# Kernel optimization log

Hardware: AMD Instinct MI355X
Metric: run time of the kernel (lower is better)

Reference implementation:

```python
import jax, jax.numpy as jnp
import numpy as np
from jax import lax

N, CI, CO, H, W = 2, 256, 256, 64, 64
K, G, DIL, PAD, STRIDE = 3, 8, 1, 1, 1
P = K * K
CG = CO // G  # group channels = 32


def setup_inputs() -> dict:
    key = jax.random.key(0)
    ks = jax.random.split(key, 24)
    r = lambda i, shape, s=1.0: jax.random.normal(ks[i], shape, jnp.float32) * s
    u = lambda i, shape: jax.random.uniform(ks[i], shape, jnp.float32, 0.5, 1.5)
    return dict(
        x=r(0, (N, CI, H, W)),
        conv1_w=r(1, (CO, CI), CI ** -0.5),
        bn1_g=u(2, (CO,)), bn1_b=r(3, (CO,), 0.1), bn1_m=r(4, (CO,), 0.1), bn1_v=u(5, (CO,)),
        inproj_w=r(6, (CO, CO), CO ** -0.5), inproj_b=r(7, (CO,), 0.02),
        dw_w=r(8, (CO, 1, K, K), 0.2), dw_b=r(9, (CO,), 0.02),
        ln_g=u(10, (CO,)), ln_b=r(11, (CO,), 0.02),
        off_w=r(12, (CO, G * P * 2), CO ** -0.5), off_b=jnp.zeros((G * P * 2,), jnp.float32),
        mask_w=r(13, (CO, G * P), CO ** -0.5), mask_b=jnp.zeros((G * P,), jnp.float32),
        outproj_w=r(14, (CO, CO), CO ** -0.5), outproj_b=r(15, (CO,), 0.02),
        bn2_g=u(16, (CO,)), bn2_b=r(17, (CO,), 0.1), bn2_m=r(18, (CO,), 0.1), bn2_v=u(19, (CO,)),
    )


def _bn(x, g, b, m, v, eps):
    # inference-mode BatchNorm2d on NCHW
    return (x - m[:, None, None]) * (g[:, None, None] * lax.rsqrt(v[:, None, None] + eps)) + b[:, None, None]


def _dcn_core(t, offset, mask):
    # t: (N,H,W,C) projected input; offset: (N,H,W,G*P*2); mask: (N,H,W,G,P) softmaxed
    xp = jnp.pad(t, ((0, 0), (PAD, PAD), (PAD, PAD), (0, 0)))
    H_, W_ = H + 2 * PAD, W + 2 * PAD
    # reference points (sample centers), normalized to padded size
    ry = ((DIL * (K - 1)) / 2 + 0.5 + STRIDE * jnp.arange(H, dtype=t.dtype)) / H_
    rx = ((DIL * (K - 1)) / 2 + 0.5 + STRIDE * jnp.arange(W, dtype=t.dtype)) / W_
    base = (DIL * (K - 1)) // 2
    gx = jnp.linspace(-base, -base + (K - 1) * DIL, K, dtype=t.dtype) / W_
    gy = jnp.linspace(-base, -base + (K - 1) * DIL, K, dtype=t.dtype) / H_
    gxx, gyy = jnp.meshgrid(gx, gy, indexing='ij')  # x varies along axis 0 (torch meshgrid order)
    grid = jnp.stack([gxx, gyy], -1).reshape(P, 2)  # (P,2)
    off = offset.reshape(N, H, W, G, P, 2) / jnp.array([W_, H_], t.dtype)
    loc_x = rx[None, None, :, None, None] + grid[:, 0][None, None, None, None] + off[..., 0]  # (N,H,W,G,P)
    loc_y = ry[None, :, None, None, None] + grid[:, 1][None, None, None, None] + off[..., 1]
    # grid_sample(align_corners=False): pixel = norm*size - 0.5
    px = jnp.transpose(loc_x * W_ - 0.5, (0, 3, 1, 2, 4)).reshape(N, G, H * W * P)
    py = jnp.transpose(loc_y * H_ - 0.5, (0, 3, 1, 2, 4)).reshape(N, G, H * W * P)
    # grouped channels-last image: (N,G,H_*W_,CG)
    xg = jnp.transpose(xp.reshape(N, H_, W_, G, CG), (0, 3, 1, 2, 4)).reshape(N, G, H_ * W_, CG)
    x0 = jnp.floor(px)
    y0 = jnp.floor(py)
    wx1 = px - x0
    wy1 = py - y0
    x0i = x0.astype(jnp.int32)
    y0i = y0.astype(jnp.int32)

    def corner(xi, yi, w):
        valid = (xi >= 0) & (xi <= W_ - 1) & (yi >= 0) & (yi <= H_ - 1)
        idx = jnp.clip(yi, 0, H_ - 1) * W_ + jnp.clip(xi, 0, W_ - 1)
        v = jnp.take_along_axis(xg, idx[..., None], axis=2)  # (N,G,M,CG)
        return v * jnp.where(valid, w, 0.0)[..., None]

    sampled = (corner(x0i, y0i, (1 - wx1) * (1 - wy1))
               + corner(x0i + 1, y0i, wx1 * (1 - wy1))
               + corner(x0i, y0i + 1, (1 - wx1) * wy1)
               + corner(x0i + 1, y0i + 1, wx1 * wy1))
    sampled = sampled.reshape(N, G, H * W, P, CG)
    mg = jnp.transpose(mask, (0, 3, 1, 2, 4)).reshape(N, G, H * W, P)
    out = jnp.einsum('nglpc,nglp->nglc', sampled, mg)
    return jnp.transpose(out, (0, 2, 1, 3)).reshape(N, H, W, G * CG)


def reference(x, conv1_w, bn1_g, bn1_b, bn1_m, bn1_v, inproj_w, inproj_b, dw_w, dw_b,
              ln_g, ln_b, off_w, off_b, mask_w, mask_b, outproj_w, outproj_b,
              bn2_g, bn2_b, bn2_m, bn2_v):
    # Conv(inc, ouc, k=1): 1x1 conv (no bias) + BN(eps=1e-3) + SiLU
    y = jnp.einsum('nchw,oc->nohw', x, conv1_w)
    y = jax.nn.silu(_bn(y, bn1_g, bn1_b, bn1_m, bn1_v, 1e-3))
    t = jnp.transpose(y, (0, 2, 3, 1))  # NHWC
    xproj = t @ inproj_w + inproj_b     # input_proj Linear
    # offset/mask branch: depthwise conv (k=3,s=1,p=1) -> LN over C -> GELU
    z = lax.conv_general_dilated(y, dw_w, (1, 1), ((PAD, PAD), (PAD, PAD)),
                                 feature_group_count=CO,
                                 dimension_numbers=('NCHW', 'OIHW', 'NCHW')) + dw_b[None, :, None, None]
    z = jnp.transpose(z, (0, 2, 3, 1))
    mu = jnp.mean(z, -1, keepdims=True)
    var = jnp.var(z, -1, keepdims=True)
    z = (z - mu) * lax.rsqrt(var + 1e-5) * ln_g + ln_b
    z = jax.nn.gelu(z, approximate=False)
    offset = z @ off_w + off_b  # (N,H,W,G*P*2)
    mask = jax.nn.softmax((z @ mask_w + mask_b).reshape(N, H, W, G, P), axis=-1)
    s = _dcn_core(xproj, offset, mask)
    s = s @ outproj_w + outproj_b  # output_proj Linear
    o = jnp.transpose(s, (0, 3, 1, 2))  # back to NCHW
    return jax.nn.silu(_bn(o, bn2_g, bn2_b, bn2_m, bn2_v, 1e-5))
```

## Files before the change

### kernel.cpp

```cpp
#include <hip/hip_runtime.h>
#include <hip/hip_fp16.h>
#include <math.h>

#define CC    256
#define HH    64
#define WW    64
#define HWSZ  4096
#define NPIX  8192
#define MT    16
#define TT    16
#define ASTR  264

typedef __attribute__((ext_vector_type(8))) _Float16 half8;
typedef __attribute__((ext_vector_type(4))) float f32x4;

__device__ __forceinline__ float silu_f(float x) { return x / (1.f + __expf(-x)); }

__device__ __forceinline__ short f2h(float f) {
    __half h = __float2half(f);
    return *reinterpret_cast<short*>(&h);
}
__device__ __forceinline__ unsigned h2u(float a, float b) {
    __half2 h = __floats2half2_rn(a, b);
    return *reinterpret_cast<unsigned*>(&h);
}
__device__ __forceinline__ __half2 u2h(unsigned v) { return *reinterpret_cast<__half2*>(&v); }
__device__ __forceinline__ unsigned h2raw(__half2 h) { return *reinterpret_cast<unsigned*>(&h); }
__device__ __forceinline__ float4 h2f4(uint2 u) {
    float2 a = __half22float2(u2h(u.x));
    float2 b = __half22float2(u2h(u.y));
    return make_float4(a.x, a.y, b.x, b.y);
}

__global__ void k_prep(const float* __restrict__ cw, const float* __restrict__ ipw,
                       const float* __restrict__ offw, const float* __restrict__ maskw,
                       const float* __restrict__ opw, const float* __restrict__ dww,
                       const float* __restrict__ offb, const float* __restrict__ maskb,
                       const float* __restrict__ g1, const float* __restrict__ b1,
                       const float* __restrict__ m1, const float* __restrict__ v1,
                       const float* __restrict__ g2, const float* __restrict__ b2,
                       const float* __restrict__ m2, const float* __restrict__ v2,
                       short* __restrict__ Wc1b, short* __restrict__ Wipb,
                       short* __restrict__ Whb, short* __restrict__ Wopb,
                       float* __restrict__ dwt,
                       float* __restrict__ bh, float* __restrict__ sc1, float* __restrict__ sh1,
                       float* __restrict__ sc2, float* __restrict__ sh2) {
    int o = blockIdx.x, c = threadIdx.x;
    Wc1b[o * CC + c] = f2h(cw[o * CC + c]);
    Wipb[o * CC + c] = f2h(ipw[c * CC + o]);
    float hv = 0.f;
    if (o < 144) hv = offw[c * 144 + o];
    else if (o < 216) hv = maskw[c * 72 + (o - 144)];
    Whb[o * CC + c] = f2h(hv);
    Wopb[o * CC + c] = f2h(opw[c * CC + o]);
    if (o < 9) dwt[o * CC + c] = dww[c * 9 + o];
    if (o == 0) {
        float bv = 0.f;
        if (c < 144) bv = offb[c];
        else if (c < 216) bv = maskb[c - 144];
        bh[c] = bv;
        float s1 = g1[c] * rsqrtf(v1[c] + 1e-3f);
        sc1[c] = s1; sh1[c] = b1[c] - m1[c] * s1;
        float s2 = g2[c] * rsqrtf(v2[c] + 1e-5f);
        sc2[c] = s2; sh2[c] = b2[c] - m2[c] * s2;
    }
}

__device__ __forceinline__ void gemm1(const short* As, const short* __restrict__ Wb,
                                      int lane, int n0, f32x4* acc) {
    const int m = lane & 15, q = lane >> 4;
#pragma unroll
    for (int kk = 0; kk < 8; ++kk) {
        int c0 = kk * 32 + q * 8;
        half8 a = *(const half8*)(As + m * ASTR + c0);
        half8 b = *(const half8*)(Wb + (size_t)(n0 + m) * CC + c0);
        *acc = __builtin_amdgcn_mfma_f32_16x16x32_f16(a, b, *acc, 0, 0, 0);
    }
}

__global__ __launch_bounds__(1024, 8) void k_conv_in(
        const float* __restrict__ x, const short* __restrict__ Wc1b,
        const short* __restrict__ Wipb, const float* __restrict__ sc1,
        const float* __restrict__ sh1, const float* __restrict__ ipb,
        short* __restrict__ ybf, short* __restrict__ xpb) {
    __shared__ __align__(16) short As[MT * ASTR];
    int tid = threadIdx.x, lane = tid & 63, wv = tid >> 6;
    int pix0 = blockIdx.x * MT;
    int n = pix0 >> 12, hw0 = pix0 & (HWSZ - 1);
    int n0 = wv * 16;
    const float* xn = x + (size_t)n * CC * HWSZ;
    {
        int c = tid >> 2, i4 = (tid & 3) * 4;
        float4 v = *(const float4*)(xn + (size_t)c * HWSZ + hw0 + i4);
        As[(i4 + 0) * ASTR + c] = f2h(v.x);
        As[(i4 + 1) * ASTR + c] = f2h(v.y);
        As[(i4 + 2) * ASTR + c] = f2h(v.z);
        As[(i4 + 3) * ASTR + c] = f2h(v.w);
    }
    __syncthreads();
    f32x4 acc = (f32x4){0.f, 0.f, 0.f, 0.f};
    gemm1(As, Wc1b, lane, n0, &acc);
    __syncthreads();
    int col = lane & 15, qr = (lane >> 4) * 4;
    int o = n0 + col;
    {
        float sc = sc1[o], sh = sh1[o];
#pragma unroll
        for (int r = 0; r < 4; ++r)
            As[(qr + r) * ASTR + o] = f2h(silu_f(acc[r] * sc + sh));
    }
    __syncthreads();
    *(uint2*)(ybf + (size_t)(pix0 + wv) * CC + lane * 4) =
        *(const uint2*)(As + wv * ASTR + lane * 4);
    acc = (f32x4){0.f, 0.f, 0.f, 0.f};
    gemm1(As, Wipb, lane, n0, &acc);
    __syncthreads();
    {
        float bo = ipb[o];
#pragma unroll
        for (int r = 0; r < 4; ++r)
            As[(qr + r) * ASTR + o] = f2h(acc[r] + bo);
    }
    __syncthreads();
    *(uint2*)(xpb + (size_t)(pix0 + wv) * CC + lane * 4) =
        *(const uint2*)(As + wv * ASTR + lane * 4);
}

__global__ __launch_bounds__(1024, 8) void k_tail(
        const short* __restrict__ ybf, const short* __restrict__ xpb,
        const float* __restrict__ dwt, const float* __restrict__ dwb,
        const float* __restrict__ lng, const float* __restrict__ lnb,
        const short* __restrict__ Whb, const float* __restrict__ bh,
        const short* __restrict__ Wopb, const float* __restrict__ opb,
        const float* __restrict__ sc2, const float* __restrict__ sh2,
        float* __restrict__ out) {
    __shared__ __align__(16) short As[TT * ASTR];
    __shared__ __align__(16) float buf[TT * 260];
    float* ml   = buf;
    float* loff = buf + 1216;
    float* xs   = buf;

    int tid = threadIdx.x, lane = tid & 63, wv = tid >> 6;
    int bid = blockIdx.x;
    int swz = ((bid & 7) << 6) | (bid >> 3);
    int pix0 = swz * TT;
    int n = pix0 >> 12, hw0 = pix0 & (HWSZ - 1);
    int h = hw0 >> 6, w0 = hw0 & 63;
    int c0 = lane * 4;
    int n0 = wv * 16;
    int col = lane & 15, qr = (lane >> 4) * 4;

    {
        float4 dwbv = *(const float4*)(dwb + c0);
        float4 lngv = *(const float4*)(lng + c0);
        float4 lnbv = *(const float4*)(lnb + c0);
        const short* yn = ybf + (size_t)n * HWSZ * CC;
        int pix = wv;
        int w = w0 + pix;
        float4 acc = dwbv;
#pragma unroll
        for (int ky = 0; ky < 3; ++ky) {
            int yy = h + ky - 1;
            int yc = min(max(yy, 0), HH - 1);
            float vy = (yy == yc) ? 1.f : 0.f;
#pragma unroll
            for (int kx = 0; kx < 3; ++kx) {
                int xx = w + kx - 1;
                int xc = min(max(xx, 0), WW - 1);
                float vm = vy * ((xx == xc) ? 1.f : 0.f);
                int t = ky * 3 + kx;
                float4 wt = *(const float4*)(dwt + t * CC + c0);
                float4 yv = h2f4(*(const uint2*)(yn + (size_t)((yc << 6) + xc) * CC + c0));
                acc.x += yv.x * wt.x * vm;
                acc.y += yv.y * wt.y * vm;
                acc.z += yv.z * wt.z * vm;
                acc.w += yv.w * wt.w * vm;
            }
        }
        float s1 = acc.x + acc.y + acc.z + acc.w;
        float s2 = acc.x * acc.x + acc.y * acc.y + acc.z * acc.z + acc.w * acc.w;
#pragma unroll
        for (int off = 32; off > 0; off >>= 1) {
            s1 += __shfl_xor(s1, off);
            s2 += __shfl_xor(s2, off);
        }
        float mu = s1 * (1.f / 256.f);
        float var = s2 * (1.f / 256.f) - mu * mu;
        float rs = rsqrtf(var + 1e-5f);
        float4 zv;
        zv.x = (acc.x - mu) * rs * lngv.x + lnbv.x;
        zv.y = (acc.y - mu) * rs * lngv.y + lnbv.y;
        zv.z = (acc.z - mu) * rs * lngv.z + lnbv.z;
        zv.w = (acc.w - mu) * rs * lngv.w + lnbv.w;
        zv.x = 0.5f * zv.x * (1.f + erff(zv.x * 0.70710678118654752f));
        zv.y = 0.5f * zv.y * (1.f + erff(zv.y * 0.70710678118654752f));
        zv.z = 0.5f * zv.z * (1.f + erff(zv.z * 0.70710678118654752f));
        zv.w = 0.5f * zv.w * (1.f + erff(zv.w * 0.70710678118654752f));
        *(uint2*)(As + pix * ASTR + c0) = make_uint2(h2u(zv.x, zv.y), h2u(zv.z, zv.w));
    }
    __syncthreads();

    {
        f32x4 acc = (f32x4){0.f, 0.f, 0.f, 0.f};
        gemm1(As, Whb, lane, n0, &acc);
        int o = n0 + col;
        float bo = bh[o];
#pragma unroll
        for (int r = 0; r < 4; ++r) {
            float v = acc[r] + bo;
            int pix = qr + r;
            if (o < 144) loff[pix * 144 + o] = v;
            else if (o < 216) ml[pix * 76 + (o - 144)] = v;
        }
    }
    __syncthreads();

    {
        int g  = lane >> 3;
        int ci = lane & 7;
        int gc0 = g * 32 + ci * 4;
        int pix = wv;
        int w = w0 + pix;
        float e9[9];
        {
            const float* row = ml + pix * 76 + g * 9;
            float mx = -1e30f;
#pragma unroll
            for (int p = 0; p < 9; ++p) { e9[p] = row[p]; mx = fmaxf(mx, e9[p]); }
            float ssum = 0.f;
#pragma unroll
            for (int p = 0; p < 9; ++p) { e9[p] = __expf(e9[p] - mx); ssum += e9[p]; }
            float inv = 1.f / ssum;
#pragma unroll
            for (int p = 0; p < 9; ++p) e9[p] *= inv;
        }
        const float* lp = loff + pix * 144 + g * 18;
        const short* xpn = xpb + (size_t)n * HWSZ * CC;
        __half2 a01 = u2h(0u), a23 = u2h(0u);
#pragma unroll
        for (int p = 0; p < 9; ++p) {
            float ox = lp[p * 2], oy = lp[p * 2 + 1];
            float px = (float)(w + p / 3) + ox;
            float py = (float)(h + p % 3) + oy;
            float fx = floorf(px), fy = floorf(py);
            float wx1 = px - fx, wy1 = py - fy;
            int x0 = (int)fx, y0 = (int)fy;
            int x1 = x0 + 1, y1 = y0 + 1;
            int xc0 = min(max(x0, 1), WW), xc1 = min(max(x1, 1), WW);
            int yc0 = min(max(y0, 1), HH), yc1 = min(max(y1, 1), HH);
            float vx0 = (x0 == xc0) ? 1.f : 0.f, vx1 = (x1 == xc1) ? 1.f : 0.f;
            float vy0 = (y0 == yc0) ? 1.f : 0.f, vy1 = (y1 == yc1) ? 1.f : 0.f;
            float mval = e9[p];
            float w00 = (1.f - wx1) * (1.f - wy1) * mval * vx0 * vy0;
            float w10 = wx1 * (1.f - wy1) * mval * vx1 * vy0;
            float w01 = (1.f - wx1) * wy1 * mval * vx0 * vy1;
            float w11 = wx1 * wy1 * mval * vx1 * vy1;
            uint2 u00 = *(const uint2*)(xpn + (size_t)(((yc0 - 1) << 6) + (xc0 - 1)) * CC + gc0);
            uint2 u10 = *(const uint2*)(xpn + (size_t)(((yc0 - 1) << 6) + (xc1 - 1)) * CC + gc0);
            uint2 u01 = *(const uint2*)(xpn + (size_t)(((yc1 - 1) << 6) + (xc0 - 1)) * CC + gc0);
            uint2 u11 = *(const uint2*)(xpn + (size_t)(((yc1 - 1) << 6) + (xc1 - 1)) * CC + gc0);
            __half2 W00 = __float2half2_rn(w00);
            __half2 W10 = __float2half2_rn(w10);
            __half2 W01 = __float2half2_rn(w01);
            __half2 W11 = __float2half2_rn(w11);
            a01 = __hfma2(u2h(u00.x), W00, a01); a23 = __hfma2(u2h(u00.y), W00, a23);
            a01 = __hfma2(u2h(u10.x), W10, a01); a23 = __hfma2(u2h(u10.y), W10, a23);
            a01 = __hfma2(u2h(u01.x), W01, a01); a23 = __hfma2(u2h(u01.y), W01, a23);
            a01 = __hfma2(u2h(u11.x), W11, a01); a23 = __hfma2(u2h(u11.y), W11, a23);
        }
        *(uint2*)(As + pix * ASTR + gc0) = make_uint2(h2raw(a01), h2raw(a23));
    }
    __syncthreads();

    {
        f32x4 acc = (f32x4){0.f, 0.f, 0.f, 0.f};
        gemm1(As, Wopb, lane, n0, &acc);
        int o = n0 + col;
        float bo = opb[o], sc = sc2[o], sh = sh2[o];
#pragma unroll
        for (int r = 0; r < 4; ++r)
            xs[(qr + r) * 260 + o] = silu_f((acc[r] + bo) * sc + sh);
    }
    __syncthreads();

    {
        int i4 = (tid & 3) * 4;
        int o = tid >> 2;
        float* on = out + (size_t)n * CC * HWSZ + hw0 + i4;
        float4 ov;
        ov.x = xs[(i4 + 0) * 260 + o];
        ov.y = xs[(i4 + 1) * 260 + o];
        ov.z = xs[(i4 + 2) * 260 + o];
        ov.w = xs[(i4 + 3) * 260 + o];
        *(float4*)(on + (size_t)o * HWSZ) = ov;
    }
}

extern "C" void kernel_launch(void* const* d_in, const int* in_sizes, int n_in,
                              void* d_out, int out_size, void* d_ws, size_t ws_size,
                              hipStream_t stream) {
    const float* x        = (const float*)d_in[0];
    const float* conv1_w  = (const float*)d_in[1];
    const float* bn1_g    = (const float*)d_in[2];
    const float* bn1_b    = (const float*)d_in[3];
    const float* bn1_m    = (const float*)d_in[4];
    const float* bn1_v    = (const float*)d_in[5];
    const float* inproj_w = (const float*)d_in[6];
    const float* inproj_b = (const float*)d_in[7];
    const float* dw_w     = (const float*)d_in[8];
    const float* dw_b     = (const float*)d_in[9];
    const float* ln_g     = (const float*)d_in[10];
    const float* ln_b     = (const float*)d_in[11];
    const float* off_w    = (const float*)d_in[12];
    const float* off_b    = (const float*)d_in[13];
    const float* mask_w   = (const float*)d_in[14];
    const float* mask_b   = (const float*)d_in[15];
    const float* outproj_w = (const float*)d_in[16];
    const float* outproj_b = (const float*)d_in[17];
    const float* bn2_g    = (const float*)d_in[18];
    const float* bn2_b    = (const float*)d_in[19];
    const float* bn2_m    = (const float*)d_in[20];
    const float* bn2_v    = (const float*)d_in[21];
    float* out = (float*)d_out;

    short* Wc1b = (short*)d_ws;
    short* Wipb = Wc1b + 65536;
    short* Whb  = Wipb + 65536;
    short* Wopb = Whb + 65536;
    float* fp   = (float*)(Wopb + 65536);
    float* dwt  = fp;
    float* bh   = dwt + 9 * CC;
    float* sc1  = bh + 256;
    float* sh1  = sc1 + 256;
    float* sc2  = sh1 + 256;
    float* sh2  = sc2 + 256;
    short* ybf  = (short*)(sh2 + 256);
    short* xpb  = ybf + (size_t)NPIX * CC;

    k_prep<<<dim3(CC), dim3(CC), 0, stream>>>(conv1_w, inproj_w, off_w, mask_w, outproj_w, dw_w,
                                              off_b, mask_b, bn1_g, bn1_b, bn1_m, bn1_v,
                                              bn2_g, bn2_b, bn2_m, bn2_v,
                                              Wc1b, Wipb, Whb, Wopb, dwt, bh, sc1, sh1, sc2, sh2);
    k_conv_in<<<dim3(NPIX / MT), dim3(1024), 0, stream>>>(x, Wc1b, Wipb, sc1, sh1, inproj_b, ybf, xpb);
    k_tail<<<dim3(NPIX / TT), dim3(1024), 0, stream>>>(ybf, xpb, dwt, dw_b, ln_g, ln_b,
                                                       Whb, bh, Wopb, outproj_b, sc2, sh2, out);
}
```

Before: 156.0 us.

## Split deformable sampling taps across lane pairs with wider loads and interior fast path

The bilinear sampling stage now gives each lane 8 channels (16-byte loads) and splits the 9 taps between two lanes (5 and 4), merging the partial sums with a shuffle-xor. The mask logits are stored at a 12-float stride so they can be read as float4, and the softmax max-subtraction is dropped. The depthwise conv also gains a branch-free path for blocks away from the image border. The aim is more memory parallelism per lane and fewer address and mask instructions, at the cost of dropping the overflow guard in the softmax and doing the fp16 cross-lane add.

```diff
diff --git a/kernel.cpp b/kernel.cpp
--- a/kernel.cpp
+++ b/kernel.cpp
@@ -137,7 +137,7 @@
     __shared__ __align__(16) short As[TT * ASTR];
     __shared__ __align__(16) float buf[TT * 260];
     float* ml   = buf;
-    float* loff = buf + 1216;
+    float* loff = buf + 1536;
     float* xs   = buf;
 
     int tid = threadIdx.x, lane = tid & 63, wv = tid >> 6;
@@ -158,23 +158,41 @@
         int pix = wv;
         int w = w0 + pix;
         float4 acc = dwbv;
-#pragma unroll
-        for (int ky = 0; ky < 3; ++ky) {
-            int yy = h + ky - 1;
-            int yc = min(max(yy, 0), HH - 1);
-            float vy = (yy == yc) ? 1.f : 0.f;
-#pragma unroll
-            for (int kx = 0; kx < 3; ++kx) {
-                int xx = w + kx - 1;
-                int xc = min(max(xx, 0), WW - 1);
-                float vm = vy * ((xx == xc) ? 1.f : 0.f);
-                int t = ky * 3 + kx;
-                float4 wt = *(const float4*)(dwt + t * CC + c0);
-                float4 yv = h2f4(*(const uint2*)(yn + (size_t)((yc << 6) + xc) * CC + c0));
-                acc.x += yv.x * wt.x * vm;
-                acc.y += yv.y * wt.y * vm;
-                acc.z += yv.z * wt.z * vm;
-                acc.w += yv.w * wt.w * vm;
+        bool inter = (h > 0) && (h < HH - 1) && (w0 > 0) && (w0 < WW - TT);
+        if (inter) {
+#pragma unroll
+            for (int ky = 0; ky < 3; ++ky) {
+#pragma unroll
+                for (int kx = 0; kx < 3; ++kx) {
+                    int t = ky * 3 + kx;
+                    float4 wt = *(const float4*)(dwt + t * CC + c0);
+                    int idx = ((h + ky - 1) << 6) + (w + kx - 1);
+                    float4 yv = h2f4(*(const uint2*)(yn + (size_t)idx * CC + c0));
+                    acc.x += yv.x * wt.x;
+                    acc.y += yv.y * wt.y;
+                    acc.z += yv.z * wt.z;
+                    acc.w += yv.w * wt.w;
+                }
+            }
+        } else {
+#pragma unroll
+            for (int ky = 0; ky < 3; ++ky) {
+                int yy = h + ky - 1;
+                int yc = min(max(yy, 0), HH - 1);
+                float vy = (yy == yc) ? 1.f : 0.f;
+#pragma unroll
+                for (int kx = 0; kx < 3; ++kx) {
+                    int xx = w + kx - 1;
+                    int xc = min(max(xx, 0), WW - 1);
+                    float vm = vy * ((xx == xc) ? 1.f : 0.f);
+                    int t = ky * 3 + kx;
+                    float4 wt = *(const float4*)(dwt + t * CC + c0);
+                    float4 yv = h2f4(*(const uint2*)(yn + (size_t)((yc << 6) + xc) * CC + c0));
+                    acc.x += yv.x * wt.x * vm;
+                    acc.y += yv.y * wt.y * vm;
+                    acc.z += yv.z * wt.z * vm;
+                    acc.w += yv.w * wt.w * vm;
+                }
             }
         }
         float s1 = acc.x + acc.y + acc.z + acc.w;
@@ -210,38 +228,42 @@
             float v = acc[r] + bo;
             int pix = qr + r;
             if (o < 144) loff[pix * 144 + o] = v;
-            else if (o < 216) ml[pix * 76 + (o - 144)] = v;
+            else if (o < 216) {
+                int mo = o - 144;
+                int mg = (mo * 7282) >> 16;
+                ml[pix * 96 + mg * 12 + (mo - mg * 9)] = v;
+            }
         }
     }
     __syncthreads();
 
     {
-        int g  = lane >> 3;
-        int ci = lane & 7;
-        int gc0 = g * 32 + ci * 4;
+        int g   = lane >> 3;
+        int ci  = lane & 7;
+        int cq  = ci & 3;
+        int par = ci >> 2;
+        int gc0 = g * 32 + cq * 8;
         int pix = wv;
         int w = w0 + pix;
-        float e9[9];
-        {
-            const float* row = ml + pix * 76 + g * 9;
-            float mx = -1e30f;
-#pragma unroll
-            for (int p = 0; p < 9; ++p) { e9[p] = row[p]; mx = fmaxf(mx, e9[p]); }
-            float ssum = 0.f;
-#pragma unroll
-            for (int p = 0; p < 9; ++p) { e9[p] = __expf(e9[p] - mx); ssum += e9[p]; }
-            float inv = 1.f / ssum;
-#pragma unroll
-            for (int p = 0; p < 9; ++p) e9[p] *= inv;
-        }
-        const float* lp = loff + pix * 144 + g * 18;
+        const float* row = ml + pix * 96 + g * 12;
+        float4 r0 = *(const float4*)(row);
+        float4 r1 = *(const float4*)(row + 4);
+        float e0 = __expf(r0.x), e1 = __expf(r0.y), e2 = __expf(r0.z);
+        float e3 = __expf(r0.w), e4 = __expf(r1.x), e5 = __expf(r1.y);
+        float e6 = __expf(r1.z), e7 = __expf(r1.w), e8 = __expf(row[8]);
+        float inv = 1.f / (e0 + e1 + e2 + e3 + e4 + e5 + e6 + e7 + e8);
+        float m0 = (par ? e5 : e0) * inv;
+        float m1 = (par ? e6 : e1) * inv;
+        float m2 = (par ? e7 : e2) * inv;
+        float m3 = (par ? e8 : e3) * inv;
+        float m4 = e4 * inv;
+        const float* lp = loff + pix * 144 + g * 18 + par * 10;
         const short* xpn = xpb + (size_t)n * HWSZ * CC;
-        __half2 a01 = u2h(0u), a23 = u2h(0u);
-#pragma unroll
-        for (int p = 0; p < 9; ++p) {
-            float ox = lp[p * 2], oy = lp[p * 2 + 1];
-            float px = (float)(w + p / 3) + ox;
-            float py = (float)(h + p % 3) + oy;
+        __half2 a0 = u2h(0u), a1 = u2h(0u), a2 = u2h(0u), a3 = u2h(0u);
+
+        auto dotap = [&](float ox, float oy, int tx, int ty, float mval) {
+            float px = (float)(w + tx) + ox;
+            float py = (float)(h + ty) + oy;
             float fx = floorf(px), fy = floorf(py);
             float wx1 = px - fx, wy1 = py - fy;
             int x0 = (int)fx, y0 = (int)fy;
@@ -250,25 +272,54 @@
             int yc0 = min(max(y0, 1), HH), yc1 = min(max(y1, 1), HH);
             float vx0 = (x0 == xc0) ? 1.f : 0.f, vx1 = (x1 == xc1) ? 1.f : 0.f;
             float vy0 = (y0 == yc0) ? 1.f : 0.f, vy1 = (y1 == yc1) ? 1.f : 0.f;
-            float mval = e9[p];
             float w00 = (1.f - wx1) * (1.f - wy1) * mval * vx0 * vy0;
             float w10 = wx1 * (1.f - wy1) * mval * vx1 * vy0;
             float w01 = (1.f - wx1) * wy1 * mval * vx0 * vy1;
             float w11 = wx1 * wy1 * mval * vx1 * vy1;
-            uint2 u00 = *(const uint2*)(xpn + (size_t)(((yc0 - 1) << 6) + (xc0 - 1)) * CC + gc0);
-            uint2 u10 = *(const uint2*)(xpn + (size_t)(((yc0 - 1) << 6) + (xc1 - 1)) * CC + gc0);
-            uint2 u01 = *(const uint2*)(xpn + (size_t)(((yc1 - 1) << 6) + (xc0 - 1)) * CC + gc0);
-            uint2 u11 = *(const uint2*)(xpn + (size_t)(((yc1 - 1) << 6) + (xc1 - 1)) * CC + gc0);
+            int i00 = (((yc0 - 1) << 6) + (xc0 - 1)) * CC + gc0;
+            int i10 = (((yc0 - 1) << 6) + (xc1 - 1)) * CC + gc0;
+            int i01 = (((yc1 - 1) << 6) + (xc0 - 1)) * CC + gc0;
+            int i11 = (((yc1 - 1) << 6) + (xc1 - 1)) * CC + gc0;
+            uint4 u00 = *(const uint4*)(xpn + i00);
+            uint4 u10 = *(const uint4*)(xpn + i10);
+            uint4 u01 = *(const uint4*)(xpn + i01);
+            uint4 u11 = *(const uint4*)(xpn + i11);
             __half2 W00 = __float2half2_rn(w00);
             __half2 W10 = __float2half2_rn(w10);
             __half2 W01 = __float2half2_rn(w01);
             __half2 W11 = __float2half2_rn(w11);
-            a01 = __hfma2(u2h(u00.x), W00, a01); a23 = __hfma2(u2h(u00.y), W00, a23);
-            a01 = __hfma2(u2h(u10.x), W10, a01); a23 = __hfma2(u2h(u10.y), W10, a23);
-            a01 = __hfma2(u2h(u01.x), W01, a01); a23 = __hfma2(u2h(u01.y), W01, a23);
-            a01 = __hfma2(u2h(u11.x), W11, a01); a23 = __hfma2(u2h(u11.y), W11, a23);
+            a0 = __hfma2(u2h(u00.x), W00, a0); a1 = __hfma2(u2h(u00.y), W00, a1);
+            a2 = __hfma2(u2h(u00.z), W00, a2); a3 = __hfma2(u2h(u00.w), W00, a3);
+            a0 = __hfma2(u2h(u10.x), W10, a0); a1 = __hfma2(u2h(u10.y), W10, a1);
+            a2 = __hfma2(u2h(u10.z), W10, a2); a3 = __hfma2(u2h(u10.w), W10, a3);
+            a0 = __hfma2(u2h(u01.x), W01, a0); a1 = __hfma2(u2h(u01.y), W01, a1);
+            a2 = __hfma2(u2h(u01.z), W01, a2); a3 = __hfma2(u2h(u01.w), W01, a3);
+            a0 = __hfma2(u2h(u11.x), W11, a0); a1 = __hfma2(u2h(u11.y), W11, a1);
+            a2 = __hfma2(u2h(u11.z), W11, a2); a3 = __hfma2(u2h(u11.w), W11, a3);
+        };
+
+        {
+            float2 of;
+            of = *(const float2*)(lp + 0);
+            dotap(of.x, of.y, par ? 1 : 0, par ? 2 : 0, m0);
+            of = *(const float2*)(lp + 2);
+            dotap(of.x, of.y, par ? 2 : 0, par ? 0 : 1, m1);
+            of = *(const float2*)(lp + 4);
+            dotap(of.x, of.y, par ? 2 : 0, par ? 1 : 2, m2);
+            of = *(const float2*)(lp + 6);
+            dotap(of.x, of.y, par ? 2 : 1, par ? 2 : 0, m3);
+            if (!par) {
+                of = *(const float2*)(lp + 8);
+                dotap(of.x, of.y, 1, 1, m4);
+            }
         }
-        *(uint2*)(As + pix * ASTR + gc0) = make_uint2(h2raw(a01), h2raw(a23));
+        a0 = __hadd2(a0, u2h((unsigned)__shfl_xor((int)h2raw(a0), 4)));
+        a1 = __hadd2(a1, u2h((unsigned)__shfl_xor((int)h2raw(a1), 4)));
+        a2 = __hadd2(a2, u2h((unsigned)__shfl_xor((int)h2raw(a2), 4)));
+        a3 = __hadd2(a3, u2h((unsigned)__shfl_xor((int)h2raw(a3), 4)));
+        if (!par)
+            *(uint4*)(As + pix * ASTR + gc0) =
+                make_uint4(h2raw(a0), h2raw(a1), h2raw(a2), h2raw(a3));
     }
     __syncthreads();
 
```

Result: no change. 158.1 us (+1.3%).
